# Performance work log

Hardware: AMD Instinct MI355X
Metric: run time of the kernel (lower is better)

Reference implementation:

```python
import jax, jax.numpy as jnp
import numpy as np

B, S_SRC, S_TGT = 32, 64, 1024
D, H, DFF, LE, LD, V = 128, 8, 512, 6, 6, 64


def _pe(S, d):
    # PyTorch-style sinusoidal positional encoding, shape [S, d]
    pos = np.arange(S, dtype=np.float32)[:, None]
    div = np.exp(np.arange(0, d, 2, dtype=np.float32) * (-np.log(10000.0) / d))
    pe = np.zeros((S, d), dtype=np.float32)
    pe[:, 0::2] = np.sin(pos * div)
    pe[:, 1::2] = np.cos(pos * div)
    return jnp.asarray(pe)


def _ln(x, g, b, eps=1e-5):
    m = x.mean(-1, keepdims=True)
    v = ((x - m) ** 2).mean(-1, keepdims=True)
    return (x - m) / jnp.sqrt(v + eps) * g + b


def _mha(q_in, k_in, v_in, Wqkv, bqkv, Wo, bo):
    d = q_in.shape[-1]
    dh = d // H
    def proj(x, W, b):
        return (x @ W.T + b).reshape(x.shape[0], x.shape[1], H, dh)
    q = proj(q_in, Wqkv[:d], bqkv[:d])
    k = proj(k_in, Wqkv[d:2 * d], bqkv[d:2 * d])
    v = proj(v_in, Wqkv[2 * d:], bqkv[2 * d:])
    scores = jnp.einsum('bqhd,bkhd->bhqk', q, k) * (1.0 / np.sqrt(dh))
    a = jax.nn.softmax(scores, axis=-1)
    o = jnp.einsum('bhqk,bkhd->bqhd', a, v).reshape(q_in.shape[0], q_in.shape[1], d)
    return o @ Wo.T + bo


def _ffn(x, W1, b1, W2, b2):
    return jax.nn.relu(x @ W1.T + b1) @ W2.T + b2


def reference(src, tgt, emb,
              enc_qkv_w, enc_qkv_b, enc_out_w, enc_out_b,
              enc_ln1_g, enc_ln1_b, enc_ff1_w, enc_ff1_b,
              enc_ff2_w, enc_ff2_b, enc_ln2_g, enc_ln2_b,
              enc_norm_g, enc_norm_b,
              dec_sa_qkv_w, dec_sa_qkv_b, dec_sa_out_w, dec_sa_out_b,
              dec_ln1_g, dec_ln1_b,
              dec_ca_qkv_w, dec_ca_qkv_b, dec_ca_out_w, dec_ca_out_b,
              dec_ln2_g, dec_ln2_b,
              dec_ff1_w, dec_ff1_b, dec_ff2_w, dec_ff2_b,
              dec_ln3_g, dec_ln3_b, dec_norm_g, dec_norm_b,
              fc_w, fc_b):
    # src: [B, S_SRC] int tokens (occupation config); tgt: [B, S_TGT, D] (zeros in the original)
    s = emb[src] * np.sqrt(float(D)) + _pe(src.shape[1], D)
    t = tgt + _pe(tgt.shape[1], D)
    # encoder (post-norm, ReLU, dropout=0 in eval)
    for i in range(LE):
        s = _ln(s + _mha(s, s, s, enc_qkv_w[i], enc_qkv_b[i], enc_out_w[i], enc_out_b[i]),
                enc_ln1_g[i], enc_ln1_b[i])
        s = _ln(s + _ffn(s, enc_ff1_w[i], enc_ff1_b[i], enc_ff2_w[i], enc_ff2_b[i]),
                enc_ln2_g[i], enc_ln2_b[i])
    mem = _ln(s, enc_norm_g, enc_norm_b)
    # decoder
    for i in range(LD):
        t = _ln(t + _mha(t, t, t, dec_sa_qkv_w[i], dec_sa_qkv_b[i], dec_sa_out_w[i], dec_sa_out_b[i]),
                dec_ln1_g[i], dec_ln1_b[i])
        t = _ln(t + _mha(t, mem, mem, dec_ca_qkv_w[i], dec_ca_qkv_b[i], dec_ca_out_w[i], dec_ca_out_b[i]),
                dec_ln2_g[i], dec_ln2_b[i])
        t = _ln(t + _ffn(t, dec_ff1_w[i], dec_ff1_b[i], dec_ff2_w[i], dec_ff2_b[i]),
                dec_ln3_g[i], dec_ln3_b[i])
    t = _ln(t, dec_norm_g, dec_norm_b)
    return t @ fc_w.T + fc_b  # [B, S_TGT, 1] transformer correction to TN params


def setup_inputs():
    ks = iter(jax.random.split(jax.random.key(0), 64))
    def nrm(shape, scale=0.02):
        return jax.random.normal(next(ks), shape, dtype=jnp.float32) * scale
    inp = {
        'src': jax.random.randint(next(ks), (B, S_SRC), 0, V),
        'tgt': jnp.zeros((B, S_TGT, D), jnp.float32),
        'emb': nrm((V, D), 1.0),
        'enc_qkv_w': nrm((LE, 3 * D, D)), 'enc_qkv_b': jnp.zeros((LE, 3 * D)),
        'enc_out_w': nrm((LE, D, D)), 'enc_out_b': jnp.zeros((LE, D)),
        'enc_ln1_g': jnp.ones((LE, D)), 'enc_ln1_b': jnp.zeros((LE, D)),
        'enc_ff1_w': nrm((LE, DFF, D)), 'enc_ff1_b': jnp.zeros((LE, DFF)),
        'enc_ff2_w': nrm((LE, D, DFF)), 'enc_ff2_b': jnp.zeros((LE, D)),
        'enc_ln2_g': jnp.ones((LE, D)), 'enc_ln2_b': jnp.zeros((LE, D)),
        'enc_norm_g': jnp.ones((D,)), 'enc_norm_b': jnp.zeros((D,)),
        'dec_sa_qkv_w': nrm((LD, 3 * D, D)), 'dec_sa_qkv_b': jnp.zeros((LD, 3 * D)),
        'dec_sa_out_w': nrm((LD, D, D)), 'dec_sa_out_b': jnp.zeros((LD, D)),
        'dec_ln1_g': jnp.ones((LD, D)), 'dec_ln1_b': jnp.zeros((LD, D)),
        'dec_ca_qkv_w': nrm((LD, 3 * D, D)), 'dec_ca_qkv_b': jnp.zeros((LD, 3 * D)),
        'dec_ca_out_w': nrm((LD, D, D)), 'dec_ca_out_b': jnp.zeros((LD, D)),
        'dec_ln2_g': jnp.ones((LD, D)), 'dec_ln2_b': jnp.zeros((LD, D)),
        'dec_ff1_w': nrm((LD, DFF, D)), 'dec_ff1_b': jnp.zeros((LD, DFF)),
        'dec_ff2_w': nrm((LD, D, DFF)), 'dec_ff2_b': jnp.zeros((LD, D)),
        'dec_ln3_g': jnp.ones((LD, D)), 'dec_ln3_b': jnp.zeros((LD, D)),
        'dec_norm_g': jnp.ones((D,)), 'dec_norm_b': jnp.zeros((D,)),
        'fc_w': nrm((1, D)), 'fc_b': jnp.zeros((1,)),
    }
    return inp
```

## Files before the change

### kernel.cpp

```cpp
#include <hip/hip_runtime.h>
#include <hip/hip_bf16.h>
#include <stdint.h>

#define NH 8

typedef uint16_t u16;
typedef uint32_t u32;
typedef __attribute__((ext_vector_type(8))) short s8b;
typedef __attribute__((ext_vector_type(4))) float f32x4;
typedef __attribute__((ext_vector_type(16))) float f32x16;

#if __has_builtin(__builtin_amdgcn_exp2f)
#define EXPS(x) __builtin_amdgcn_exp2f(x)
#define QSCALE 0.36067376022224085f
#else
#define EXPS(x) __expf(x)
#define QSCALE 0.25f
#endif

__device__ __forceinline__ u16 f2b(float f) {
    u32 u = __builtin_bit_cast(u32, f);
    u = (u + 0x7fffu + ((u >> 16) & 1u)) >> 16;
    return (u16)u;
}

__device__ __forceinline__ u32 pkbf(float a, float b) {
    u32 ua = __builtin_bit_cast(u32, a) + 0x8000u;
    u32 ub = __builtin_bit_cast(u32, b) + 0x8000u;
    return __builtin_amdgcn_perm(ub, ua, 0x07060302);
}

__device__ __forceinline__ float pe_val(int pos, int d) {
    int j = d >> 1;
    float div = expf((float)j * -0.14391156831212787f);
    float ang = (float)pos * div;
    return (d & 1) ? cosf(ang) : sinf(ang);
}

__global__ void embed_kernel(const int* __restrict__ src, const float* __restrict__ emb,
                             float* __restrict__ S, u16* __restrict__ Sb) {
    int idx = blockIdx.x * 256 + threadIdx.x;
    int d = idx & 127;
    int n = idx >> 7;
    int i = n & 63;
    int tok = src[n];
    float v = emb[tok * 128 + d] * 11.313708498984761f + pe_val(i, d);
    S[idx] = v; Sb[idx] = f2b(v);
}

__global__ void addpe_kernel(const float* __restrict__ tgt, float* __restrict__ T,
                             u16* __restrict__ Tb) {
    int idx = blockIdx.x * 256 + threadIdx.x;
    int d = idx & 127;
    int n = idx >> 7;
    int i = n & 1023;
    float v = tgt[idx] + pe_val(i, d);
    T[idx] = v; Tb[idx] = f2b(v);
}

struct CvtJobs { const float* src[10]; u16* dst[10]; int n[10]; };
__global__ void cvt_kernel(CvtJobs jb) {
    int e = blockIdx.y;
    int i = blockIdx.x * 256 + threadIdx.x;
    if (i < jb.n[e]) jb.dst[e][i] = f2b(jb.src[e][i]);
}

__global__ void transposeV(const u16* __restrict__ KV, int stride, int voff,
                           u16* __restrict__ VT, int SKV) {
    int bh = blockIdx.x;
    int k0 = blockIdx.y * 64;
    int l = threadIdx.x;
    int b = bh >> 3, h = bh & 7;
    const u16* p = KV + (size_t)(b * SKV + k0 + l) * stride + voff + h * 16;
    s8b v0 = *(const s8b*)p;
    s8b v1 = *(const s8b*)(p + 8);
    size_t obase = (size_t)bh * 16 * SKV + k0 + l;
#pragma unroll
    for (int n = 0; n < 8; n++) VT[obase + (size_t)n * SKV] = (u16)v0[n];
#pragma unroll
    for (int n = 0; n < 8; n++) VT[obase + (size_t)(n + 8) * SKV] = (u16)v1[n];
}

template <int RELU>
__global__ __launch_bounds__(256) void gemm_mfma(const u16* __restrict__ A,
                                                 const u16* __restrict__ W,
                                                 const float* __restrict__ bias,
                                                 u16* __restrict__ C,
                                                 int M, int N, int K,
                                                 float qscale, int qcols) {
    __shared__ __align__(16) u16 As[128 * 56];
    __shared__ __align__(16) u16 Bs[128 * 56];
    int tid = threadIdx.x;
    int lane = tid & 63, w = tid >> 6;
    int quad = lane >> 4, l15 = lane & 15;
    int m0 = blockIdx.y * 128, n0 = blockIdx.x * 128;
    int wm = (w & 1) * 64, wn = (w >> 1) * 64;
    int srow = tid >> 1, skof = (tid & 1) * 16;

    f32x4 acc[4][4];
#pragma unroll
    for (int i = 0; i < 4; i++)
#pragma unroll
        for (int j = 0; j < 4; j++)
#pragma unroll
            for (int r = 0; r < 4; r++) acc[i][j][r] = 0.f;

    for (int k0 = 0; k0 < K; k0 += 32) {
        const u16* ga = A + (size_t)(m0 + srow) * K + k0 + skof;
        const u16* gw = W + (size_t)(n0 + srow) * K + k0 + skof;
        s8b a0 = *(const s8b*)ga, a1 = *(const s8b*)(ga + 8);
        s8b w0 = *(const s8b*)gw, w1 = *(const s8b*)(gw + 8);
        __syncthreads();
        *(s8b*)(As + srow * 56 + skof) = a0;
        *(s8b*)(As + srow * 56 + skof + 8) = a1;
        *(s8b*)(Bs + srow * 56 + skof) = w0;
        *(s8b*)(Bs + srow * 56 + skof + 8) = w1;
        __syncthreads();
        s8b af[4], bfr[4];
#pragma unroll
        for (int i = 0; i < 4; i++) af[i] = *(const s8b*)(As + (wm + 16 * i + l15) * 56 + quad * 8);
#pragma unroll
        for (int j = 0; j < 4; j++) bfr[j] = *(const s8b*)(Bs + (wn + 16 * j + l15) * 56 + quad * 8);
#pragma unroll
        for (int i = 0; i < 4; i++)
#pragma unroll
            for (int j = 0; j < 4; j++)
                acc[i][j] = __builtin_amdgcn_mfma_f32_16x16x32_bf16(af[i], bfr[j], acc[i][j], 0, 0, 0);
    }
#pragma unroll
    for (int j = 0; j < 4; j++) {
        int col = n0 + wn + 16 * j + l15;
        float bv = bias[col];
        float sc = (col < qcols) ? qscale : 1.f;
#pragma unroll
        for (int i = 0; i < 4; i++) {
            int rbase = m0 + wm + 16 * i + quad * 4;
#pragma unroll
            for (int r = 0; r < 4; r++) {
                float v = (acc[i][j][r] + bv) * sc;
                if (RELU) v = fmaxf(v, 0.f);
                C[(size_t)(rbase + r) * N + col] = f2b(v);
            }
        }
    }
}

__global__ __launch_bounds__(256) void gemm_ln(const u16* __restrict__ A,
                                               const u16* __restrict__ W,
                                               const float* __restrict__ bias,
                                               const float* __restrict__ X,
                                               const float* __restrict__ g,
                                               const float* __restrict__ bta,
                                               float* __restrict__ Y,
                                               u16* __restrict__ Yb,
                                               int M, int K) {
    __shared__ __align__(16) u16 As[128 * 56];
    __shared__ __align__(16) u16 Bs[128 * 56];
    __shared__ float redS[128][2], redQ[128][2];
    int tid = threadIdx.x;
    int lane = tid & 63, w = tid >> 6;
    int quad = lane >> 4, l15 = lane & 15;
    int m0 = blockIdx.x * 128;
    int wm = (w & 1) * 64, wn = (w >> 1) * 64;
    int srow = tid >> 1, skof = (tid & 1) * 16;

    f32x4 acc[4][4];
#pragma unroll
    for (int i = 0; i < 4; i++)
#pragma unroll
        for (int j = 0; j < 4; j++)
#pragma unroll
            for (int r = 0; r < 4; r++) acc[i][j][r] = 0.f;

    for (int k0 = 0; k0 < K; k0 += 32) {
        const u16* ga = A + (size_t)(m0 + srow) * K + k0 + skof;
        const u16* gw = W + (size_t)srow * K + k0 + skof;
        s8b a0 = *(const s8b*)ga, a1 = *(const s8b*)(ga + 8);
        s8b w0 = *(const s8b*)gw, w1 = *(const s8b*)(gw + 8);
        __syncthreads();
        *(s8b*)(As + srow * 56 + skof) = a0;
        *(s8b*)(As + srow * 56 + skof + 8) = a1;
        *(s8b*)(Bs + srow * 56 + skof) = w0;
        *(s8b*)(Bs + srow * 56 + skof + 8) = w1;
        __syncthreads();
        s8b af[4], bfr[4];
#pragma unroll
        for (int i = 0; i < 4; i++) af[i] = *(const s8b*)(As + (wm + 16 * i + l15) * 56 + quad * 8);
#pragma unroll
        for (int j = 0; j < 4; j++) bfr[j] = *(const s8b*)(Bs + (wn + 16 * j + l15) * 56 + quad * 8);
#pragma unroll
        for (int i = 0; i < 4; i++)
#pragma unroll
            for (int j = 0; j < 4; j++)
                acc[i][j] = __builtin_amdgcn_mfma_f32_16x16x32_bf16(af[i], bfr[j], acc[i][j], 0, 0, 0);
    }

    float s_[4][4], q_[4][4];
#pragma unroll
    for (int i = 0; i < 4; i++)
#pragma unroll
        for (int r = 0; r < 4; r++) {
            int row = m0 + wm + 16 * i + quad * 4 + r;
            float s = 0.f, q = 0.f;
#pragma unroll
            for (int j = 0; j < 4; j++) {
                int col = wn + 16 * j + l15;
                float x = acc[i][j][r] + bias[col] + X[(size_t)row * 128 + col];
                acc[i][j][r] = x;
                s += x; q += x * x;
            }
#pragma unroll
            for (int off = 1; off < 16; off <<= 1) {
                s += __shfl_xor(s, off);
                q += __shfl_xor(q, off);
            }
            s_[i][r] = s; q_[i][r] = q;
        }
    if (l15 == 0) {
#pragma unroll
        for (int i = 0; i < 4; i++)
#pragma unroll
            for (int r = 0; r < 4; r++) {
                int lrow = wm + 16 * i + quad * 4 + r;
                redS[lrow][wn >> 6] = s_[i][r];
                redQ[lrow][wn >> 6] = q_[i][r];
            }
    }
    __syncthreads();
#pragma unroll
    for (int i = 0; i < 4; i++)
#pragma unroll
        for (int r = 0; r < 4; r++) {
            int lrow = wm + 16 * i + quad * 4 + r;
            int row = m0 + lrow;
            float S2 = redS[lrow][0] + redS[lrow][1];
            float Q2 = redQ[lrow][0] + redQ[lrow][1];
            float mean = S2 * (1.f / 128.f);
            float var = Q2 * (1.f / 128.f) - mean * mean;
            float rstd = rsqrtf(var + 1e-5f);
#pragma unroll
            for (int j = 0; j < 4; j++) {
                int col = wn + 16 * j + l15;
                float y = (acc[i][j][r] - mean) * rstd * g[col] + bta[col];
                Y[(size_t)row * 128 + col] = y;
                Yb[(size_t)row * 128 + col] = f2b(y);
            }
        }
}

template <int WAVES>
__global__ __launch_bounds__(WAVES * 64) void attn3(
    const u16* __restrict__ Qb, int qstride, int qoff,
    const u16* __restrict__ Kb, int kstride, int koff,
    const u16* __restrict__ VT,
    u16* __restrict__ O, int SQ, int SKV) {
    __shared__ __align__(16) u32 Ps[WAVES][32 * 20];
    int tid = threadIdx.x;
    int lane = tid & 63, w = tid >> 6;
    int quad = lane >> 4, l15 = lane & 15, l31 = lane & 31, half = lane >> 5;
    int nqc = SQ / (WAVES * 32);
    int bid = blockIdx.x;
    int qc = bid % nqc;
    int h = (bid / nqc) % NH;
    int b = bid / (nqc * NH);
    int q0 = qc * WAVES * 32 + w * 32;

    const u16* qp = Qb + (size_t)(b * SQ + q0 + l31) * qstride + qoff + h * 16 + half * 8;
    s8b qf = *(const s8b*)qp;
    s8b ones;
#pragma unroll
    for (int j = 0; j < 8; j++) ones[j] = (short)0x3F80;

    const u16* vtb = VT + ((size_t)(b * NH + h) * 16 + l15) * SKV + quad * 8;
    const u16* kp = Kb + (size_t)(b * SKV + l31) * kstride + koff + h * 16 + half * 8;
    size_t kadv = (size_t)32 * kstride;

    f32x4 O0, O1, L0, L1;
#pragma unroll
    for (int r = 0; r < 4; r++) { O0[r] = 0.f; O1[r] = 0.f; L0[r] = 0.f; L1[r] = 0.f; }

    u32* pw = Ps[w];
#pragma unroll 2
    for (int j0 = 0; j0 < SKV; j0 += 32) {
        s8b kf = *(const s8b*)kp;
        kp += kadv;
        s8b vb = *(const s8b*)(vtb + j0);
        f32x16 S;
#pragma unroll
        for (int r = 0; r < 16; r++) S[r] = 0.f;
        S = __builtin_amdgcn_mfma_f32_32x32x16_bf16(kf, qf, S, 0, 0, 0);
#pragma unroll
        for (int g = 0; g < 4; g++) {
            float p0 = EXPS(S[4 * g + 0]);
            float p1 = EXPS(S[4 * g + 1]);
            float p2 = EXPS(S[4 * g + 2]);
            float p3 = EXPS(S[4 * g + 3]);
            int kw = l31 * 20 + 2 * half + 4 * g;
            pw[kw] = pkbf(p0, p1);
            pw[kw + 1] = pkbf(p2, p3);
        }
        __builtin_amdgcn_wave_barrier();
        s8b pa0 = *(const s8b*)(pw + l15 * 20 + quad * 4);
        s8b pa1 = *(const s8b*)(pw + (16 + l15) * 20 + quad * 4);
        O0 = __builtin_amdgcn_mfma_f32_16x16x32_bf16(pa0, vb, O0, 0, 0, 0);
        O1 = __builtin_amdgcn_mfma_f32_16x16x32_bf16(pa1, vb, O1, 0, 0, 0);
        L0 = __builtin_amdgcn_mfma_f32_16x16x32_bf16(pa0, ones, L0, 0, 0, 0);
        L1 = __builtin_amdgcn_mfma_f32_16x16x32_bf16(pa1, ones, L1, 0, 0, 0);
    }
#pragma unroll
    for (int r = 0; r < 4; r++) {
        int q = b * SQ + q0 + quad * 4 + r;
        O[(size_t)q * 128 + h * 16 + l15] = f2b(O0[r] / L0[r]);
        O[(size_t)(q + 16) * 128 + h * 16 + l15] = f2b(O1[r] / L1[r]);
    }
}

__global__ void ln_kernel(const float* __restrict__ X, const float* __restrict__ R,
                          const float* __restrict__ g, const float* __restrict__ bta,
                          float* __restrict__ Y, u16* __restrict__ Yb) {
    int r = blockIdx.x;
    int lane = threadIdx.x;
    size_t base = (size_t)r * 128;
    float x0 = X[base + lane], x1 = X[base + lane + 64];
    if (R) { x0 += R[base + lane]; x1 += R[base + lane + 64]; }
    float s = x0 + x1;
    for (int off = 32; off; off >>= 1) s += __shfl_xor(s, off);
    float mean = s * (1.f / 128.f);
    float d0 = x0 - mean, d1 = x1 - mean;
    float vs = d0 * d0 + d1 * d1;
    for (int off = 32; off; off >>= 1) vs += __shfl_xor(vs, off);
    float rstd = rsqrtf(vs * (1.f / 128.f) + 1e-5f);
    float y0 = d0 * rstd * g[lane] + bta[lane];
    float y1 = d1 * rstd * g[lane + 64] + bta[lane + 64];
    Y[base + lane] = y0;
    Y[base + lane + 64] = y1;
    if (Yb) { Yb[base + lane] = f2b(y0); Yb[base + lane + 64] = f2b(y1); }
}

__global__ void fc_kernel(const float* __restrict__ X, const float* __restrict__ w,
                          const float* __restrict__ b, float* __restrict__ out) {
    int r = blockIdx.x;
    int lane = threadIdx.x;
    size_t base = (size_t)r * 128;
    float s = X[base + lane] * w[lane] + X[base + lane + 64] * w[lane + 64];
    for (int off = 32; off; off >>= 1) s += __shfl_xor(s, off);
    if (lane == 0) out[r] = s + b[0];
}

static inline void gemm_b(const u16* A, const u16* W, const float* bias, u16* C,
                          int M, int N, int K, hipStream_t st, int qcols = 0) {
    hipLaunchKernelGGL((gemm_mfma<0>), dim3(N / 128, M / 128), dim3(256), 0, st,
                       A, W, bias, C, M, N, K, QSCALE, qcols);
}
static inline void gemm_br(const u16* A, const u16* W, const float* bias, u16* C,
                           int M, int N, int K, hipStream_t st) {
    hipLaunchKernelGGL((gemm_mfma<1>), dim3(N / 128, M / 128), dim3(256), 0, st,
                       A, W, bias, C, M, N, K, 1.f, 0);
}
static inline void gemmln(const u16* A, const u16* W, const float* bias,
                          const float* X, const float* g, const float* bta,
                          float* Y, u16* Yb, int M, int K, hipStream_t st) {
    hipLaunchKernelGGL(gemm_ln, dim3(M / 128), dim3(256), 0, st,
                       A, W, bias, X, g, bta, Y, Yb, M, K);
}

extern "C" void kernel_launch(void* const* d_in, const int* in_sizes, int n_in,
                              void* d_out, int out_size, void* d_ws, size_t ws_size,
                              hipStream_t stream) {
    const int B = 32, SSRC = 64, STGT = 1024, D = 128, DFF_ = 512, LE = 6, LD = 6;

    const int*   src = (const int*)d_in[0];
    const float* tgt = (const float*)d_in[1];
    const float* emb = (const float*)d_in[2];
    const float* enc_qkv_w = (const float*)d_in[3];
    const float* enc_qkv_b = (const float*)d_in[4];
    const float* enc_out_w = (const float*)d_in[5];
    const float* enc_out_b = (const float*)d_in[6];
    const float* enc_ln1_g = (const float*)d_in[7];
    const float* enc_ln1_b = (const float*)d_in[8];
    const float* enc_ff1_w = (const float*)d_in[9];
    const float* enc_ff1_b = (const float*)d_in[10];
    const float* enc_ff2_w = (const float*)d_in[11];
    const float* enc_ff2_b = (const float*)d_in[12];
    const float* enc_ln2_g = (const float*)d_in[13];
    const float* enc_ln2_b = (const float*)d_in[14];
    const float* enc_norm_g = (const float*)d_in[15];
    const float* enc_norm_b = (const float*)d_in[16];
    const float* dec_sa_qkv_w = (const float*)d_in[17];
    const float* dec_sa_qkv_b = (const float*)d_in[18];
    const float* dec_sa_out_w = (const float*)d_in[19];
    const float* dec_sa_out_b = (const float*)d_in[20];
    const float* dec_ln1_g = (const float*)d_in[21];
    const float* dec_ln1_b = (const float*)d_in[22];
    const float* dec_ca_qkv_w = (const float*)d_in[23];
    const float* dec_ca_qkv_b = (const float*)d_in[24];
    const float* dec_ca_out_w = (const float*)d_in[25];
    const float* dec_ca_out_b = (const float*)d_in[26];
    const float* dec_ln2_g = (const float*)d_in[27];
    const float* dec_ln2_b = (const float*)d_in[28];
    const float* dec_ff1_w = (const float*)d_in[29];
    const float* dec_ff1_b = (const float*)d_in[30];
    const float* dec_ff2_w = (const float*)d_in[31];
    const float* dec_ff2_b = (const float*)d_in[32];
    const float* dec_ln3_g = (const float*)d_in[33];
    const float* dec_ln3_b = (const float*)d_in[34];
    const float* dec_norm_g = (const float*)d_in[35];
    const float* dec_norm_b = (const float*)d_in[36];
    const float* fc_w = (const float*)d_in[37];
    const float* fc_b = (const float*)d_in[38];

    const int NT = B * STGT;
    const int NS = B * SSRC;

    float* t_f   = (float*)d_ws;
    float* s_f   = t_f + (size_t)NT * D;
    float* mem_f = s_f + (size_t)NS * D;
    u16* t_bf    = (u16*)(mem_f + (size_t)NS * D);
    u16* s_bf    = t_bf + (size_t)NT * D;
    u16* mem_bf  = s_bf + (size_t)NS * D;
    u16* qkv_bf  = mem_bf + (size_t)NS * D;
    u16* attno_bf = qkv_bf + (size_t)NT * DFF_;
    u16* ckv_bf  = attno_bf + (size_t)NT * D;
    u16* vt      = ckv_bf + (size_t)NS * 2 * D;
    u16* wa      = vt + (size_t)B * NH * 16 * STGT;

    u16* w_enc_qkv = wa;                          int n_enc_qkv = LE * 3 * D * D;
    u16* w_enc_out = w_enc_qkv + n_enc_qkv;       int n_enc_out = LE * D * D;
    u16* w_enc_ff1 = w_enc_out + n_enc_out;       int n_enc_ff1 = LE * DFF_ * D;
    u16* w_enc_ff2 = w_enc_ff1 + n_enc_ff1;       int n_enc_ff2 = LE * D * DFF_;
    u16* w_sa_qkv  = w_enc_ff2 + n_enc_ff2;       int n_sa_qkv = LD * 3 * D * D;
    u16* w_sa_out  = w_sa_qkv + n_sa_qkv;         int n_sa_out = LD * D * D;
    u16* w_ca_qkv  = w_sa_out + n_sa_out;         int n_ca_qkv = LD * 3 * D * D;
    u16* w_ca_out  = w_ca_qkv + n_ca_qkv;         int n_ca_out = LD * D * D;
    u16* w_ff1     = w_ca_out + n_ca_out;         int n_ff1 = LD * DFF_ * D;
    u16* w_ff2     = w_ff1 + n_ff1;               int n_ff2 = LD * D * DFF_;

    float* scf = (float*)qkv_bf;

    CvtJobs jb;
    jb.src[0] = enc_qkv_w;    jb.dst[0] = w_enc_qkv; jb.n[0] = n_enc_qkv;
    jb.src[1] = enc_out_w;    jb.dst[1] = w_enc_out; jb.n[1] = n_enc_out;
    jb.src[2] = enc_ff1_w;    jb.dst[2] = w_enc_ff1; jb.n[2] = n_enc_ff1;
    jb.src[3] = enc_ff2_w;    jb.dst[3] = w_enc_ff2; jb.n[3] = n_enc_ff2;
    jb.src[4] = dec_sa_qkv_w; jb.dst[4] = w_sa_qkv;  jb.n[4] = n_sa_qkv;
    jb.src[5] = dec_sa_out_w; jb.dst[5] = w_sa_out;  jb.n[5] = n_sa_out;
    jb.src[6] = dec_ca_qkv_w; jb.dst[6] = w_ca_qkv;  jb.n[6] = n_ca_qkv;
    jb.src[7] = dec_ca_out_w; jb.dst[7] = w_ca_out;  jb.n[7] = n_ca_out;
    jb.src[8] = dec_ff1_w;    jb.dst[8] = w_ff1;     jb.n[8] = n_ff1;
    jb.src[9] = dec_ff2_w;    jb.dst[9] = w_ff2;     jb.n[9] = n_ff2;
    int maxn = n_enc_ff1;
    hipLaunchKernelGGL(cvt_kernel, dim3((maxn + 255) / 256, 10), dim3(256), 0, stream, jb);

    hipLaunchKernelGGL(embed_kernel, dim3(NS * D / 256), dim3(256), 0, stream, src, emb, s_f, s_bf);

    for (int i = 0; i < LE; i++) {
        gemm_b(s_bf, w_enc_qkv + (size_t)i * 3 * D * D, enc_qkv_b + (size_t)i * 3 * D,
               qkv_bf, NS, 3 * D, D, stream, 128);
        hipLaunchKernelGGL(transposeV, dim3(B * NH, 1), dim3(64), 0, stream,
                           qkv_bf, 3 * D, 2 * D, vt, SSRC);
        hipLaunchKernelGGL((attn3<2>), dim3(B * NH), dim3(128), 0, stream,
                           qkv_bf, 3 * D, 0, qkv_bf, 3 * D, D, vt, attno_bf, SSRC, SSRC);
        gemmln(attno_bf, w_enc_out + (size_t)i * D * D, enc_out_b + (size_t)i * D,
               s_f, enc_ln1_g + (size_t)i * D, enc_ln1_b + (size_t)i * D, s_f, s_bf, NS, D, stream);
        gemm_br(s_bf, w_enc_ff1 + (size_t)i * DFF_ * D, enc_ff1_b + (size_t)i * DFF_,
                qkv_bf, NS, DFF_, D, stream);
        gemmln(qkv_bf, w_enc_ff2 + (size_t)i * D * DFF_, enc_ff2_b + (size_t)i * D,
               s_f, enc_ln2_g + (size_t)i * D, enc_ln2_b + (size_t)i * D, s_f, s_bf, NS, DFF_, stream);
    }
    hipLaunchKernelGGL(ln_kernel, dim3(NS), dim3(64), 0, stream,
                       s_f, (const float*)nullptr, enc_norm_g, enc_norm_b, mem_f, mem_bf);

    hipLaunchKernelGGL(addpe_kernel, dim3(NT * D / 256), dim3(256), 0, stream, tgt, t_f, t_bf);

    for (int i = 0; i < LD; i++) {
        gemm_b(t_bf, w_sa_qkv + (size_t)i * 3 * D * D, dec_sa_qkv_b + (size_t)i * 3 * D,
               qkv_bf, NT, 3 * D, D, stream, 128);
        hipLaunchKernelGGL(transposeV, dim3(B * NH, STGT / 64), dim3(64), 0, stream,
                           qkv_bf, 3 * D, 2 * D, vt, STGT);
        hipLaunchKernelGGL((attn3<4>), dim3(B * NH * (STGT / 128)), dim3(256), 0, stream,
                           qkv_bf, 3 * D, 0, qkv_bf, 3 * D, D, vt, attno_bf, STGT, STGT);
        gemmln(attno_bf, w_sa_out + (size_t)i * D * D, dec_sa_out_b + (size_t)i * D,
               t_f, dec_ln1_g + (size_t)i * D, dec_ln1_b + (size_t)i * D, t_f, t_bf, NT, D, stream);

        gemm_b(t_bf, w_ca_qkv + (size_t)i * 3 * D * D, dec_ca_qkv_b + (size_t)i * 3 * D,
               qkv_bf, NT, D, D, stream, 128);
        gemm_b(mem_bf, w_ca_qkv + (size_t)i * 3 * D * D + (size_t)D * D,
               dec_ca_qkv_b + (size_t)i * 3 * D + D, ckv_bf, NS, 2 * D, D, stream);
        hipLaunchKernelGGL(transposeV, dim3(B * NH, 1), dim3(64), 0, stream,
                           ckv_bf, 2 * D, D, vt, SSRC);
        hipLaunchKernelGGL((attn3<4>), dim3(B * NH * (STGT / 128)), dim3(256), 0, stream,
                           qkv_bf, D, 0, ckv_bf, 2 * D, 0, vt, attno_bf, STGT, SSRC);
        gemmln(attno_bf, w_ca_out + (size_t)i * D * D, dec_ca_out_b + (size_t)i * D,
               t_f, dec_ln2_g + (size_t)i * D, dec_ln2_b + (size_t)i * D, t_f, t_bf, NT, D, stream);

        gemm_br(t_bf, w_ff1 + (size_t)i * DFF_ * D, dec_ff1_b + (size_t)i * DFF_,
                qkv_bf, NT, DFF_, D, stream);
        gemmln(qkv_bf, w_ff2 + (size_t)i * D * DFF_, dec_ff2_b + (size_t)i * D,
               t_f, dec_ln3_g + (size_t)i * D, dec_ln3_b + (size_t)i * D, t_f, t_bf, NT, DFF_, stream);
    }

    hipLaunchKernelGGL(ln_kernel, dim3(NT), dim3(64), 0, stream,
                       t_f, (const float*)nullptr, dec_norm_g, dec_norm_b, scf, (u16*)nullptr);
    hipLaunchKernelGGL(fc_kernel, dim3(NT), dim3(64), 0, stream,
                       scf, fc_w, fc_b, (float*)d_out);
}
```

Baseline: 1.508 ms.

## Fuse V transpose into QKV GEMM epilogue and drop fp32 residual stream

The QKV projection GEMM now writes the V columns straight into the head-transposed VT layout in its epilogue, so the separate transposeV launches go away. The fp32 residual copies are removed, and the residual stream is kept only in bf16. The LN-fused GEMMs read the bf16 residual and no longer write fp32 output. P-tile stores in attention are widened to 64-bit. This cuts launches and memory traffic, at the cost of more rounding error from keeping the residual in bf16.

```diff
diff --git a/kernel.cpp b/kernel.cpp
--- a/kernel.cpp
+++ b/kernel.cpp
@@ -6,6 +6,7 @@
 
 typedef uint16_t u16;
 typedef uint32_t u32;
+typedef __attribute__((ext_vector_type(2))) u32 u32x2;
 typedef __attribute__((ext_vector_type(8))) short s8b;
 typedef __attribute__((ext_vector_type(4))) float f32x4;
 typedef __attribute__((ext_vector_type(16))) float f32x16;
@@ -23,7 +24,9 @@
     u = (u + 0x7fffu + ((u >> 16) & 1u)) >> 16;
     return (u16)u;
 }
-
+__device__ __forceinline__ float b2f(u16 u) {
+    return __builtin_bit_cast(float, (u32)u << 16);
+}
 __device__ __forceinline__ u32 pkbf(float a, float b) {
     u32 ua = __builtin_bit_cast(u32, a) + 0x8000u;
     u32 ub = __builtin_bit_cast(u32, b) + 0x8000u;
@@ -38,24 +41,21 @@
 }
 
 __global__ void embed_kernel(const int* __restrict__ src, const float* __restrict__ emb,
-                             float* __restrict__ S, u16* __restrict__ Sb) {
+                             u16* __restrict__ Sb) {
     int idx = blockIdx.x * 256 + threadIdx.x;
     int d = idx & 127;
     int n = idx >> 7;
     int i = n & 63;
     int tok = src[n];
-    float v = emb[tok * 128 + d] * 11.313708498984761f + pe_val(i, d);
-    S[idx] = v; Sb[idx] = f2b(v);
-}
-
-__global__ void addpe_kernel(const float* __restrict__ tgt, float* __restrict__ T,
-                             u16* __restrict__ Tb) {
+    Sb[idx] = f2b(emb[tok * 128 + d] * 11.313708498984761f + pe_val(i, d));
+}
+
+__global__ void addpe_kernel(const float* __restrict__ tgt, u16* __restrict__ Tb) {
     int idx = blockIdx.x * 256 + threadIdx.x;
     int d = idx & 127;
     int n = idx >> 7;
     int i = n & 1023;
-    float v = tgt[idx] + pe_val(i, d);
-    T[idx] = v; Tb[idx] = f2b(v);
+    Tb[idx] = f2b(tgt[idx] + pe_val(i, d));
 }
 
 struct CvtJobs { const float* src[10]; u16* dst[10]; int n[10]; };
@@ -65,29 +65,12 @@
     if (i < jb.n[e]) jb.dst[e][i] = f2b(jb.src[e][i]);
 }
 
-__global__ void transposeV(const u16* __restrict__ KV, int stride, int voff,
-                           u16* __restrict__ VT, int SKV) {
-    int bh = blockIdx.x;
-    int k0 = blockIdx.y * 64;
-    int l = threadIdx.x;
-    int b = bh >> 3, h = bh & 7;
-    const u16* p = KV + (size_t)(b * SKV + k0 + l) * stride + voff + h * 16;
-    s8b v0 = *(const s8b*)p;
-    s8b v1 = *(const s8b*)(p + 8);
-    size_t obase = (size_t)bh * 16 * SKV + k0 + l;
-#pragma unroll
-    for (int n = 0; n < 8; n++) VT[obase + (size_t)n * SKV] = (u16)v0[n];
-#pragma unroll
-    for (int n = 0; n < 8; n++) VT[obase + (size_t)(n + 8) * SKV] = (u16)v1[n];
-}
-
 template <int RELU>
-__global__ __launch_bounds__(256) void gemm_mfma(const u16* __restrict__ A,
-                                                 const u16* __restrict__ W,
-                                                 const float* __restrict__ bias,
-                                                 u16* __restrict__ C,
-                                                 int M, int N, int K,
-                                                 float qscale, int qcols) {
+__global__ __launch_bounds__(256) void gemm_mfma(
+    const u16* __restrict__ A, const u16* __restrict__ W,
+    const float* __restrict__ bias, u16* __restrict__ C,
+    int M, int N, int K, float qscale, int qcols,
+    u16* __restrict__ vt, int vcol0, int sshift, int smask, int skv) {
     __shared__ __align__(16) u16 As[128 * 56];
     __shared__ __align__(16) u16 Bs[128 * 56];
     int tid = threadIdx.x;
@@ -127,6 +110,25 @@
             for (int j = 0; j < 4; j++)
                 acc[i][j] = __builtin_amdgcn_mfma_f32_16x16x32_bf16(af[i], bfr[j], acc[i][j], 0, 0, 0);
     }
+
+    if (vt && n0 == vcol0) {
+#pragma unroll
+        for (int j = 0; j < 4; j++) {
+            int lc = wn + 16 * j + l15;
+            int h = lc >> 4, n = lc & 15;
+            float bv = bias[vcol0 + lc];
+#pragma unroll
+            for (int i = 0; i < 4; i++) {
+                int row = m0 + wm + 16 * i + quad * 4;
+                int b = row >> sshift, tok = row & smask;
+                u32 lo = pkbf(acc[i][j][0] + bv, acc[i][j][1] + bv);
+                u32 hi = pkbf(acc[i][j][2] + bv, acc[i][j][3] + bv);
+                u32* p = (u32*)(vt + ((size_t)((b * 8 + h) * 16 + n)) * skv + tok);
+                p[0] = lo; p[1] = hi;
+            }
+        }
+        return;
+    }
 #pragma unroll
     for (int j = 0; j < 4; j++) {
         int col = n0 + wn + 16 * j + l15;
@@ -145,15 +147,11 @@
     }
 }
 
-__global__ __launch_bounds__(256) void gemm_ln(const u16* __restrict__ A,
-                                               const u16* __restrict__ W,
-                                               const float* __restrict__ bias,
-                                               const float* __restrict__ X,
-                                               const float* __restrict__ g,
-                                               const float* __restrict__ bta,
-                                               float* __restrict__ Y,
-                                               u16* __restrict__ Yb,
-                                               int M, int K) {
+__global__ __launch_bounds__(256) void gemm_ln(
+    const u16* __restrict__ A, const u16* __restrict__ W,
+    const float* __restrict__ bias, const u16* __restrict__ X,
+    const float* __restrict__ g, const float* __restrict__ bta,
+    u16* __restrict__ Yb, int M, int K) {
     __shared__ __align__(16) u16 As[128 * 56];
     __shared__ __align__(16) u16 Bs[128 * 56];
     __shared__ float redS[128][2], redQ[128][2];
@@ -205,7 +203,7 @@
 #pragma unroll
             for (int j = 0; j < 4; j++) {
                 int col = wn + 16 * j + l15;
-                float x = acc[i][j][r] + bias[col] + X[(size_t)row * 128 + col];
+                float x = acc[i][j][r] + bias[col] + b2f(X[(size_t)row * 128 + col]);
                 acc[i][j][r] = x;
                 s += x; q += x * x;
             }
@@ -242,7 +240,6 @@
             for (int j = 0; j < 4; j++) {
                 int col = wn + 16 * j + l15;
                 float y = (acc[i][j][r] - mean) * rstd * g[col] + bta[col];
-                Y[(size_t)row * 128 + col] = y;
                 Yb[(size_t)row * 128 + col] = f2b(y);
             }
         }
@@ -250,7 +247,7 @@
 
 template <int WAVES>
 __global__ __launch_bounds__(WAVES * 64) void attn3(
-    const u16* __restrict__ Qb, int qstride, int qoff,
+    const u16* __restrict__ Qb, int qstride,
     const u16* __restrict__ Kb, int kstride, int koff,
     const u16* __restrict__ VT,
     u16* __restrict__ O, int SQ, int SKV) {
@@ -265,7 +262,7 @@
     int b = bid / (nqc * NH);
     int q0 = qc * WAVES * 32 + w * 32;
 
-    const u16* qp = Qb + (size_t)(b * SQ + q0 + l31) * qstride + qoff + h * 16 + half * 8;
+    const u16* qp = Qb + (size_t)(b * SQ + q0 + l31) * qstride + h * 16 + half * 8;
     s8b qf = *(const s8b*)qp;
     s8b ones;
 #pragma unroll
@@ -295,9 +292,10 @@
             float p1 = EXPS(S[4 * g + 1]);
             float p2 = EXPS(S[4 * g + 2]);
             float p3 = EXPS(S[4 * g + 3]);
-            int kw = l31 * 20 + 2 * half + 4 * g;
-            pw[kw] = pkbf(p0, p1);
-            pw[kw + 1] = pkbf(p2, p3);
+            u32x2 pk;
+            pk[0] = pkbf(p0, p1);
+            pk[1] = pkbf(p2, p3);
+            *(u32x2*)(pw + l31 * 20 + 2 * half + 4 * g) = pk;
         }
         __builtin_amdgcn_wave_barrier();
         s8b pa0 = *(const s8b*)(pw + l15 * 20 + quad * 4);
@@ -315,14 +313,13 @@
     }
 }
 
-__global__ void ln_kernel(const float* __restrict__ X, const float* __restrict__ R,
-                          const float* __restrict__ g, const float* __restrict__ bta,
-                          float* __restrict__ Y, u16* __restrict__ Yb) {
+__global__ void ln_bf(const u16* __restrict__ X,
+                      const float* __restrict__ g, const float* __restrict__ bta,
+                      float* __restrict__ Yf, u16* __restrict__ Yb) {
     int r = blockIdx.x;
     int lane = threadIdx.x;
     size_t base = (size_t)r * 128;
-    float x0 = X[base + lane], x1 = X[base + lane + 64];
-    if (R) { x0 += R[base + lane]; x1 += R[base + lane + 64]; }
+    float x0 = b2f(X[base + lane]), x1 = b2f(X[base + lane + 64]);
     float s = x0 + x1;
     for (int off = 32; off; off >>= 1) s += __shfl_xor(s, off);
     float mean = s * (1.f / 128.f);
@@ -332,8 +329,7 @@
     float rstd = rsqrtf(vs * (1.f / 128.f) + 1e-5f);
     float y0 = d0 * rstd * g[lane] + bta[lane];
     float y1 = d1 * rstd * g[lane + 64] + bta[lane + 64];
-    Y[base + lane] = y0;
-    Y[base + lane + 64] = y1;
+    if (Yf) { Yf[base + lane] = y0; Yf[base + lane + 64] = y1; }
     if (Yb) { Yb[base + lane] = f2b(y0); Yb[base + lane + 64] = f2b(y1); }
 }
 
@@ -348,20 +344,22 @@
 }
 
 static inline void gemm_b(const u16* A, const u16* W, const float* bias, u16* C,
-                          int M, int N, int K, hipStream_t st, int qcols = 0) {
+                          int M, int N, int K, hipStream_t st, int qcols = 0,
+                          u16* vt = nullptr, int vcol0 = 0, int sshift = 0, int skv = 0) {
     hipLaunchKernelGGL((gemm_mfma<0>), dim3(N / 128, M / 128), dim3(256), 0, st,
-                       A, W, bias, C, M, N, K, QSCALE, qcols);
+                       A, W, bias, C, M, N, K, QSCALE, qcols, vt, vcol0, sshift,
+                       (1 << sshift) - 1, skv);
 }
 static inline void gemm_br(const u16* A, const u16* W, const float* bias, u16* C,
                            int M, int N, int K, hipStream_t st) {
     hipLaunchKernelGGL((gemm_mfma<1>), dim3(N / 128, M / 128), dim3(256), 0, st,
-                       A, W, bias, C, M, N, K, 1.f, 0);
+                       A, W, bias, C, M, N, K, 1.f, 0, (u16*)nullptr, 0, 0, 0, 0);
 }
 static inline void gemmln(const u16* A, const u16* W, const float* bias,
-                          const float* X, const float* g, const float* bta,
-                          float* Y, u16* Yb, int M, int K, hipStream_t st) {
+                          const u16* X, const float* g, const float* bta,
+                          u16* Yb, int M, int K, hipStream_t st) {
     hipLaunchKernelGGL(gemm_ln, dim3(M / 128), dim3(256), 0, st,
-                       A, W, bias, X, g, bta, Y, Yb, M, K);
+                       A, W, bias, X, g, bta, Yb, M, K);
 }
 
 extern "C" void kernel_launch(void* const* d_in, const int* in_sizes, int n_in,
@@ -412,17 +410,14 @@
     const int NT = B * STGT;
     const int NS = B * SSRC;
 
-    float* t_f   = (float*)d_ws;
-    float* s_f   = t_f + (size_t)NT * D;
-    float* mem_f = s_f + (size_t)NS * D;
-    u16* t_bf    = (u16*)(mem_f + (size_t)NS * D);
+    u16* t_bf    = (u16*)d_ws;
     u16* s_bf    = t_bf + (size_t)NT * D;
     u16* mem_bf  = s_bf + (size_t)NS * D;
     u16* qkv_bf  = mem_bf + (size_t)NS * D;
     u16* attno_bf = qkv_bf + (size_t)NT * DFF_;
     u16* ckv_bf  = attno_bf + (size_t)NT * D;
     u16* vt      = ckv_bf + (size_t)NS * 2 * D;
-    u16* wa      = vt + (size_t)B * NH * 16 * STGT;
+    u16* wa      = vt + (size_t)B * NH * 16 * STGT + 16 * STGT;
 
     u16* w_enc_qkv = wa;                          int n_enc_qkv = LE * 3 * D * D;
     u16* w_enc_out = w_enc_qkv + n_enc_qkv;       int n_enc_out = LE * D * D;
@@ -451,56 +446,51 @@
     int maxn = n_enc_ff1;
     hipLaunchKernelGGL(cvt_kernel, dim3((maxn + 255) / 256, 10), dim3(256), 0, stream, jb);
 
-    hipLaunchKernelGGL(embed_kernel, dim3(NS * D / 256), dim3(256), 0, stream, src, emb, s_f, s_bf);
+    hipLaunchKernelGGL(embed_kernel, dim3(NS * D / 256), dim3(256), 0, stream, src, emb, s_bf);
 
     for (int i = 0; i < LE; i++) {
         gemm_b(s_bf, w_enc_qkv + (size_t)i * 3 * D * D, enc_qkv_b + (size_t)i * 3 * D,
-               qkv_bf, NS, 3 * D, D, stream, 128);
-        hipLaunchKernelGGL(transposeV, dim3(B * NH, 1), dim3(64), 0, stream,
-                           qkv_bf, 3 * D, 2 * D, vt, SSRC);
+               qkv_bf, NS, 3 * D, D, stream, 128, vt, 256, 6, SSRC);
         hipLaunchKernelGGL((attn3<2>), dim3(B * NH), dim3(128), 0, stream,
-                           qkv_bf, 3 * D, 0, qkv_bf, 3 * D, D, vt, attno_bf, SSRC, SSRC);
+                           qkv_bf, 3 * D, qkv_bf, 3 * D, D, vt, attno_bf, SSRC, SSRC);
         gemmln(attno_bf, w_enc_out + (size_t)i * D * D, enc_out_b + (size_t)i * D,
-               s_f, enc_ln1_g + (size_t)i * D, enc_ln1_b + (size_t)i * D, s_f, s_bf, NS, D, stream);
+               s_bf, enc_ln1_g + (size_t)i * D, enc_ln1_b + (size_t)i * D, s_bf, NS, D, stream);
         gemm_br(s_bf, w_enc_ff1 + (size_t)i * DFF_ * D, enc_ff1_b + (size_t)i * DFF_,
                 qkv_bf, NS, DFF_, D, stream);
         gemmln(qkv_bf, w_enc_ff2 + (size_t)i * D * DFF_, enc_ff2_b + (size_t)i * D,
-               s_f, enc_ln2_g + (size_t)i * D, enc_ln2_b + (size_t)i * D, s_f, s_bf, NS, DFF_, stream);
-    }
-    hipLaunchKernelGGL(ln_kernel, dim3(NS), dim3(64), 0, stream,
-                       s_f, (const float*)nullptr, enc_norm_g, enc_norm_b, mem_f, mem_bf);
-
-    hipLaunchKernelGGL(addpe_kernel, dim3(NT * D / 256), dim3(256), 0, stream, tgt, t_f, t_bf);
+               s_bf, enc_ln2_g + (size_t)i * D, enc_ln2_b + (size_t)i * D, s_bf, NS, DFF_, stream);
+    }
+    hipLaunchKernelGGL(ln_bf, dim3(NS), dim3(64), 0, stream,
+                       s_bf, enc_norm_g, enc_norm_b, (float*)nullptr, mem_bf);
+
+    hipLaunchKernelGGL(addpe_kernel, dim3(NT * D / 256), dim3(256), 0, stream, tgt, t_bf);
 
     for (int i = 0; i < LD; i++) {
         gemm_b(t_bf, w_sa_qkv + (size_t)i * 3 * D * D, dec_sa_qkv_b + (size_t)i * 3 * D,
-               qkv_bf, NT, 3 * D, D, stream, 128);
-        hipLaunchKernelGGL(transposeV, dim3(B * NH, STGT / 64), dim3(64), 0, stream,
-                           qkv_bf, 3 * D, 2 * D, vt, STGT);
+               qkv_bf, NT, 3 * D, D, stream, 128, vt, 256, 10, STGT);
         hipLaunchKernelGGL((attn3<4>), dim3(B * NH * (STGT / 128)), dim3(256), 0, stream,
-                           qkv_bf, 3 * D, 0, qkv_bf, 3 * D, D, vt, attno_bf, STGT, STGT);
+                           qkv_bf, 3 * D, qkv_bf, 3 * D, D, vt, attno_bf, STGT, STGT);
         gemmln(attno_bf, w_sa_out + (size_t)i * D * D, dec_sa_out_b + (size_t)i * D,
-               t_f, dec_ln1_g + (size_t)i * D, dec_ln1_b + (size_t)i * D, t_f, t_bf, NT, D, stream);
+               t_bf, dec_ln1_g + (size_t)i * D, dec_ln1_b + (size_t)i * D, t_bf, NT, D, stream);
 
         gemm_b(t_bf, w_ca_qkv + (size_t)i * 3 * D * D, dec_ca_qkv_b + (size_t)i * 3 * D,
                qkv_bf, NT, D, D, stream, 128);
         gemm_b(mem_bf, w_ca_qkv + (size_t)i * 3 * D * D + (size_t)D * D,
-               dec_ca_qkv_b + (size_t)i * 3 * D + D, ckv_bf, NS, 2 * D, D, stream);
-        hipLaunchKernelGGL(transposeV, dim3(B * NH, 1), dim3(64), 0, stream,
-                           ckv_bf, 2 * D, D, vt, SSRC);
+               dec_ca_qkv_b + (size_t)i * 3 * D + D, ckv_bf, NS, 2 * D, D, stream,
+               0, vt, 128, 6, SSRC);
         hipLaunchKernelGGL((attn3<4>), dim3(B * NH * (STGT / 128)), dim3(256), 0, stream,
-                           qkv_bf, D, 0, ckv_bf, 2 * D, 0, vt, attno_bf, STGT, SSRC);
+                           qkv_bf, D, ckv_bf, 2 * D, 0, vt, attno_bf, STGT, SSRC);
         gemmln(attno_bf, w_ca_out + (size_t)i * D * D, dec_ca_out_b + (size_t)i * D,
-               t_f, dec_ln2_g + (size_t)i * D, dec_ln2_b + (size_t)i * D, t_f, t_bf, NT, D, stream);
+               t_bf, dec_ln2_g + (size_t)i * D, dec_ln2_b + (size_t)i * D, t_bf, NT, D, stream);
 
         gemm_br(t_bf, w_ff1 + (size_t)i * DFF_ * D, dec_ff1_b + (size_t)i * DFF_,
                 qkv_bf, NT, DFF_, D, stream);
         gemmln(qkv_bf, w_ff2 + (size_t)i * D * DFF_, dec_ff2_b + (size_t)i * D,
-               t_f, dec_ln3_g + (size_t)i * D, dec_ln3_b + (size_t)i * D, t_f, t_bf, NT, DFF_, stream);
-    }
-
-    hipLaunchKernelGGL(ln_kernel, dim3(NT), dim3(64), 0, stream,
-                       t_f, (const float*)nullptr, dec_norm_g, dec_norm_b, scf, (u16*)nullptr);
+               t_bf, dec_ln3_g + (size_t)i * D, dec_ln3_b + (size_t)i * D, t_bf, NT, DFF_, stream);
+    }
+
+    hipLaunchKernelGGL(ln_bf, dim3(NT), dim3(64), 0, stream,
+                       t_bf, dec_norm_g, dec_norm_b, scf, (u16*)nullptr);
     hipLaunchKernelGGL(fc_kernel, dim3(NT), dim3(64), 0, stream,
                        scf, fc_w, fc_b, (float*)d_out);
 }
```

Measured after the change: 1.451 ms. 3.8% less time.
